# Kernel tuning notes

Measured on AMD Instinct MI355X. Metric: run time of the kernel, lower is better.

The kernel has to match this reference:

```python
import jax, jax.numpy as jnp
import numpy as np

N_NODES = 100000
IN_CH = 64
HID = 128
N_EDGES = 1600000


def sage_conv(x, src, dst, Wl, bl, Wr, num_nodes):
    # PyG SAGEConv (mean aggr): out = lin_l(mean_{j->i} x_j) + lin_r(x_i)
    msg = x[src]                                           # [E, F] gather
    agg = jax.ops.segment_sum(msg, dst, num_segments=num_nodes)   # [N, F]
    cnt = jax.ops.segment_sum(jnp.ones((src.shape[0],), x.dtype), dst,
                              num_segments=num_nodes)      # [N]
    mean = agg / jnp.maximum(cnt, 1.0)[:, None]
    return mean @ Wl.T + bl + x @ Wr.T


def setup_inputs() -> dict:
    key = jax.random.key(0)
    k1, k2, k3, k4, k5, k6, k7, k8 = jax.random.split(key, 8)
    x = jax.random.normal(k1, (N_NODES, IN_CH), dtype=jnp.float32)
    edge_index = jax.random.randint(k2, (2, N_EDGES), 0, N_NODES, dtype=jnp.int64)
    s1 = 1.0 / np.sqrt(IN_CH)
    s2 = 1.0 / np.sqrt(HID)
    Wl1 = jax.random.uniform(k3, (HID, IN_CH), jnp.float32, -s1, s1)
    bl1 = jax.random.uniform(k4, (HID,), jnp.float32, -s1, s1)
    Wr1 = jax.random.uniform(k5, (HID, IN_CH), jnp.float32, -s1, s1)
    Wl2 = jax.random.uniform(k6, (HID, HID), jnp.float32, -s2, s2)
    bl2 = jax.random.uniform(k7, (HID,), jnp.float32, -s2, s2)
    Wr2 = jax.random.uniform(k8, (HID, HID), jnp.float32, -s2, s2)
    return {"x": x, "edge_index": edge_index,
            "Wl1": Wl1, "bl1": bl1, "Wr1": Wr1,
            "Wl2": Wl2, "bl2": bl2, "Wr2": Wr2}


def reference(x, edge_index, Wl1, bl1, Wr1, Wl2, bl2, Wr2):
    src, dst = edge_index[0], edge_index[1]
    n = x.shape[0]
    h = sage_conv(x, src, dst, Wl1, bl1, Wr1, n)
    h = jax.nn.relu(h)
    # dropout p=0.2 is identity in eval/reference mode
    out = sage_conv(h, src, dst, Wl2, bl2, Wr2, n)
    return out
```

## Files before the change

### kernel.cpp

```cpp
#include <hip/hip_runtime.h>
#include <hip/hip_bf16.h>
#include <stdint.h>

#define NN 100000
#define EE 1600000
#define NBUCK 196
#define CSB 512

typedef __attribute__((ext_vector_type(4))) float f32x4;
typedef __attribute__((ext_vector_type(8))) short bf16x8;

__device__ inline ushort f2bf(float f) {
    union { float f; uint32_t u; } v; v.f = f;
    uint32_t u = v.u;
    uint32_t r = (u + 0x7fffu + ((u >> 16) & 1u)) >> 16;
    return (ushort)r;
}
__device__ inline float bflo(uint32_t u) {
    union { uint32_t u; float f; } v; v.u = u << 16; return v.f;
}
__device__ inline float bfhi(uint32_t u) {
    union { uint32_t u; float f; } v; v.u = u & 0xffff0000u; return v.f;
}

__global__ __launch_bounds__(256) void prep_kernel(
    const float* __restrict__ x, const unsigned int* __restrict__ raw,
    const float* __restrict__ Wl1, const float* __restrict__ Wr1,
    const float* __restrict__ Wl2, const float* __restrict__ Wr2,
    ushort* __restrict__ xb, ushort* __restrict__ wc1, ushort* __restrict__ wc2,
    int* __restrict__ flag, int* __restrict__ ccnt, int* __restrict__ cfill)
{
    const int gid = blockIdx.x * 256 + threadIdx.x;
    const int stride = gridDim.x * 256;

    if (gid < 4096) {
        if (raw[2 * gid + 1] != 0u) atomicOr(flag, 1);
    }
    if (gid >= 4096 && gid < 4096 + NBUCK) ccnt[gid - 4096] = 0;
    if (gid >= 4096 + NBUCK && gid < 4096 + 2 * NBUCK) cfill[gid - 4096 - NBUCK] = 0;

    const int n4 = NN * 64 / 4;
    for (int i = gid; i < n4; i += stride) {
        float4 v = *(const float4*)&x[i * 4];
        ushort o[4] = { f2bf(v.x), f2bf(v.y), f2bf(v.z), f2bf(v.w) };
        *(uint64_t*)&xb[i * 4] = *(const uint64_t*)o;
    }
    for (int i = gid; i < 128 * 128; i += stride) {
        int o = i >> 7, k = i & 127;
        float v = (k < 64) ? Wl1[o * 64 + k] : Wr1[o * 64 + (k - 64)];
        wc1[o * 128 + k] = f2bf(v);
    }
    for (int i = gid; i < 128 * 256; i += stride) {
        int o = i >> 8, k = i & 255;
        float v = (k < 128) ? Wl2[o * 128 + k] : Wr2[o * 128 + (k - 128)];
        wc2[o * 256 + k] = f2bf(v);
    }
}

__global__ __launch_bounds__(256) void coarse_hist(const void* raw, const int* flag,
                                                   int* ccnt, int E) {
    __shared__ int lh[NBUCK];
    for (int i = threadIdx.x; i < NBUCK; i += 256) lh[i] = 0;
    __syncthreads();
    int stride = gridDim.x * 256;
    if (*flag) {
        const int* p = (const int*)raw;
        for (int e = blockIdx.x * 256 + threadIdx.x; e < E; e += stride)
            atomicAdd(&lh[p[E + e] >> 9], 1);
    } else {
        const long long* p = (const long long*)raw;
        for (int e = blockIdx.x * 256 + threadIdx.x; e < E; e += stride)
            atomicAdd(&lh[((int)p[E + e]) >> 9], 1);
    }
    __syncthreads();
    for (int i = threadIdx.x; i < NBUCK; i += 256)
        if (lh[i]) atomicAdd(&ccnt[i], lh[i]);
}

__global__ void coarse_scan(const int* ccnt, int* coff, int* offsets, int E) {
    __shared__ int part[256];
    int t = threadIdx.x;
    int v[4]; int s = 0;
    #pragma unroll
    for (int j = 0; j < 4; j++) {
        int i = t * 4 + j;
        v[j] = (i < NBUCK) ? ccnt[i] : 0;
        s += v[j];
    }
    part[t] = s; __syncthreads();
    for (int off = 1; off < 256; off <<= 1) {
        int add = (t >= off) ? part[t - off] : 0;
        __syncthreads();
        part[t] += add;
        __syncthreads();
    }
    int run = part[t] - s;
    #pragma unroll
    for (int j = 0; j < 4; j++) {
        int i = t * 4 + j;
        if (i <= NBUCK) coff[i] = run;
        run += v[j];
    }
    if (t == 0) offsets[NN] = E;
}

__global__ __launch_bounds__(256) void coarse_scatter2(const void* raw, const int* flag,
                                                       const int* coff, int* cfill,
                                                       uint32_t* pbuf, int E) {
    __shared__ int lh[NBUCK];
    __shared__ int gbase[NBUCK];
    __shared__ int lfill[NBUCK];
    const int t = threadIdx.x;
    for (int i = t; i < NBUCK; i += 256) { lh[i] = 0; lfill[i] = 0; }
    __syncthreads();
    const int chunk = (E + (int)gridDim.x - 1) / (int)gridDim.x;
    const int s0 = blockIdx.x * chunk;
    const int s1 = min(E, s0 + chunk);
    const bool is32 = (*flag != 0);
    if (is32) {
        const int* p = (const int*)raw;
        for (int e = s0 + t; e < s1; e += 256) atomicAdd(&lh[p[E + e] >> 9], 1);
    } else {
        const long long* p = (const long long*)raw;
        for (int e = s0 + t; e < s1; e += 256) atomicAdd(&lh[((int)p[E + e]) >> 9], 1);
    }
    __syncthreads();
    for (int i = t; i < NBUCK; i += 256)
        gbase[i] = coff[i] + (lh[i] ? atomicAdd(&cfill[i], lh[i]) : 0);
    __syncthreads();
    if (is32) {
        const int* p = (const int*)raw;
        for (int e = s0 + t; e < s1; e += 256) {
            int sr = p[e], d = p[E + e];
            int b = d >> 9;
            int r = atomicAdd(&lfill[b], 1);
            pbuf[gbase[b] + r] = ((uint32_t)(d & 511) << 17) | (uint32_t)sr;
        }
    } else {
        const long long* p = (const long long*)raw;
        for (int e = s0 + t; e < s1; e += 256) {
            int sr = (int)p[e], d = (int)p[E + e];
            int b = d >> 9;
            int r = atomicAdd(&lfill[b], 1);
            pbuf[gbase[b] + r] = ((uint32_t)(d & 511) << 17) | (uint32_t)sr;
        }
    }
}

__global__ __launch_bounds__(512) void fine_bucket(const uint32_t* __restrict__ pbuf,
                                                   const int* __restrict__ coff,
                                                   int* __restrict__ offsets,
                                                   int* __restrict__ srcs_sort, int N) {
    __shared__ int cnt[512], sc[512], fil[512];
    const int b = blockIdx.x, t = threadIdx.x;
    const int s = coff[b], e = coff[b + 1];
    cnt[t] = 0; fil[t] = 0;
    __syncthreads();
    for (int i = s + t; i < e; i += 512) atomicAdd(&cnt[pbuf[i] >> 17], 1);
    __syncthreads();
    sc[t] = cnt[t];
    __syncthreads();
    for (int off = 1; off < 512; off <<= 1) {
        int add = (t >= off) ? sc[t - off] : 0;
        __syncthreads();
        sc[t] += add;
        __syncthreads();
    }
    const int nb0 = b * 512;
    if (nb0 + t < N) offsets[nb0 + t] = s + sc[t] - cnt[t];
    for (int i = s + t; i < e; i += 512) {
        uint32_t p = pbuf[i];
        int dl = (int)(p >> 17);
        int sr = (int)(p & 0x1FFFFu);
        int pos = s + (sc[dl] - cnt[dl]) + atomicAdd(&fil[dl], 1);
        srcs_sort[pos] = sr;
    }
}

template<int K, bool RELU, bool OUT_BF16>
__global__ __launch_bounds__(256, 8) void sage_fused(
    const int* __restrict__ offsets, const int* __restrict__ srcs,
    const ushort* __restrict__ xin, const ushort* __restrict__ Wcat,
    const float* __restrict__ bl, void* __restrict__ outv, int N)
{
    constexpr int KT = 2 * K;
    constexpr int RP = K + 8;
    __shared__ ushort mlds[32][RP];
    const int t = threadIdx.x;
    const int w = t >> 6;
    const int lane = t & 63;
    const int nb = blockIdx.x * 32;

    const int q     = lane >> 4;
    const int ql    = lane & 15;
    const int qbase = lane & 48;

    int offv = 0;
    if (lane < 9) offv = offsets[nb + w * 8 + lane];

    for (int pi = 0; pi < 2; pi++) {
        const int ln = w * 8 + pi * 4 + q;
        const int s0 = __shfl(offv, pi * 4 + q);
        const int s1 = __shfl(offv, pi * 4 + q + 1);
        const float inv = 1.0f / fmaxf((float)(s1 - s0), 1.0f);

        if (K == 64) {
            float f0=0.f, f1=0.f, f2=0.f, f3=0.f;
            for (int base = s0; base < s1; base += 16) {
                int cnt = min(16, s1 - base);
                int myidx = (base + ql < s1) ? srcs[base + ql] : 0;
                int j = 0;
                for (; j + 4 <= cnt; j += 4) {
                    int sA = __shfl(myidx, qbase + j);
                    int sB = __shfl(myidx, qbase + j + 1);
                    int sC = __shfl(myidx, qbase + j + 2);
                    int sD = __shfl(myidx, qbase + j + 3);
                    uint2 uA = *(const uint2*)&xin[(size_t)sA * 64 + ql * 4];
                    uint2 uB = *(const uint2*)&xin[(size_t)sB * 64 + ql * 4];
                    uint2 uC = *(const uint2*)&xin[(size_t)sC * 64 + ql * 4];
                    uint2 uD = *(const uint2*)&xin[(size_t)sD * 64 + ql * 4];
                    f0 += bflo(uA.x); f1 += bfhi(uA.x); f2 += bflo(uA.y); f3 += bfhi(uA.y);
                    f0 += bflo(uB.x); f1 += bfhi(uB.x); f2 += bflo(uB.y); f3 += bfhi(uB.y);
                    f0 += bflo(uC.x); f1 += bfhi(uC.x); f2 += bflo(uC.y); f3 += bfhi(uC.y);
                    f0 += bflo(uD.x); f1 += bfhi(uD.x); f2 += bflo(uD.y); f3 += bfhi(uD.y);
                }
                for (; j < cnt; j++) {
                    int s = __shfl(myidx, qbase + j);
                    uint2 u = *(const uint2*)&xin[(size_t)s * 64 + ql * 4];
                    f0 += bflo(u.x); f1 += bfhi(u.x); f2 += bflo(u.y); f3 += bfhi(u.y);
                }
            }
            ushort o[4] = { f2bf(f0 * inv), f2bf(f1 * inv), f2bf(f2 * inv), f2bf(f3 * inv) };
            *(uint64_t*)&mlds[ln][ql * 4] = *(const uint64_t*)o;
        } else {
            float f0=0.f, f1=0.f, f2=0.f, f3=0.f, f4=0.f, f5=0.f, f6=0.f, f7=0.f;
            for (int base = s0; base < s1; base += 16) {
                int cnt = min(16, s1 - base);
                int myidx = (base + ql < s1) ? srcs[base + ql] : 0;
                int j = 0;
                for (; j + 4 <= cnt; j += 4) {
                    int sA = __shfl(myidx, qbase + j);
                    int sB = __shfl(myidx, qbase + j + 1);
                    int sC = __shfl(myidx, qbase + j + 2);
                    int sD = __shfl(myidx, qbase + j + 3);
                    uint4 uA = *(const uint4*)&xin[(size_t)sA * 128 + ql * 8];
                    uint4 uB = *(const uint4*)&xin[(size_t)sB * 128 + ql * 8];
                    uint4 uC = *(const uint4*)&xin[(size_t)sC * 128 + ql * 8];
                    uint4 uD = *(const uint4*)&xin[(size_t)sD * 128 + ql * 8];
                    f0 += bflo(uA.x); f1 += bfhi(uA.x); f2 += bflo(uA.y); f3 += bfhi(uA.y);
                    f4 += bflo(uA.z); f5 += bfhi(uA.z); f6 += bflo(uA.w); f7 += bfhi(uA.w);
                    f0 += bflo(uB.x); f1 += bfhi(uB.x); f2 += bflo(uB.y); f3 += bfhi(uB.y);
                    f4 += bflo(uB.z); f5 += bfhi(uB.z); f6 += bflo(uB.w); f7 += bfhi(uB.w);
                    f0 += bflo(uC.x); f1 += bfhi(uC.x); f2 += bflo(uC.y); f3 += bfhi(uC.y);
                    f4 += bflo(uC.z); f5 += bfhi(uC.z); f6 += bflo(uC.w); f7 += bfhi(uC.w);
                    f0 += bflo(uD.x); f1 += bfhi(uD.x); f2 += bflo(uD.y); f3 += bfhi(uD.y);
                    f4 += bflo(uD.z); f5 += bfhi(uD.z); f6 += bflo(uD.w); f7 += bfhi(uD.w);
                }
                for (; j < cnt; j++) {
                    int s = __shfl(myidx, qbase + j);
                    uint4 u = *(const uint4*)&xin[(size_t)s * 128 + ql * 8];
                    f0 += bflo(u.x); f1 += bfhi(u.x); f2 += bflo(u.y); f3 += bfhi(u.y);
                    f4 += bflo(u.z); f5 += bfhi(u.z); f6 += bflo(u.w); f7 += bfhi(u.w);
                }
            }
            ushort o[8] = { f2bf(f0 * inv), f2bf(f1 * inv), f2bf(f2 * inv), f2bf(f3 * inv),
                            f2bf(f4 * inv), f2bf(f5 * inv), f2bf(f6 * inv), f2bf(f7 * inv) };
            *(uint4*)&mlds[ln][ql * 8] = *(const uint4*)o;
        }
    }
    __syncthreads();

    const int lrow = lane & 15;
    const int lgrp = lane >> 4;
    f32x4 acc[2][2];
    #pragma unroll
    for (int nt = 0; nt < 2; nt++)
        #pragma unroll
        for (int ct = 0; ct < 2; ct++)
            acc[nt][ct] = (f32x4){0.f, 0.f, 0.f, 0.f};

    #pragma unroll
    for (int ks = 0; ks < KT; ks += 32) {
        bf16x8 x0, x1;
        if (ks < K) {
            x0 = *(const bf16x8*)&mlds[lrow][ks + lgrp * 8];
            x1 = *(const bf16x8*)&mlds[16 + lrow][ks + lgrp * 8];
        } else {
            const int ac = ks - K;
            x0 = *(const bf16x8*)&xin[(size_t)(nb + lrow) * K + ac + lgrp * 8];
            x1 = *(const bf16x8*)&xin[(size_t)(nb + 16 + lrow) * K + ac + lgrp * 8];
        }
        bf16x8 wA = *(const bf16x8*)&Wcat[(size_t)(w * 32 + lrow) * KT + ks + lgrp * 8];
        bf16x8 wB = *(const bf16x8*)&Wcat[(size_t)(w * 32 + 16 + lrow) * KT + ks + lgrp * 8];
        acc[0][0] = __builtin_amdgcn_mfma_f32_16x16x32_bf16(wA, x0, acc[0][0], 0, 0, 0);
        acc[0][1] = __builtin_amdgcn_mfma_f32_16x16x32_bf16(wB, x0, acc[0][1], 0, 0, 0);
        acc[1][0] = __builtin_amdgcn_mfma_f32_16x16x32_bf16(wA, x1, acc[1][0], 0, 0, 0);
        acc[1][1] = __builtin_amdgcn_mfma_f32_16x16x32_bf16(wB, x1, acc[1][1], 0, 0, 0);
    }

    #pragma unroll
    for (int ct = 0; ct < 2; ct++) {
        const int ch0 = w * 32 + ct * 16 + lgrp * 4;
        float4 b4 = *(const float4*)&bl[ch0];
        #pragma unroll
        for (int nt = 0; nt < 2; nt++) {
            int n = nb + nt * 16 + lrow;
            float v0 = acc[nt][ct][0] + b4.x;
            float v1 = acc[nt][ct][1] + b4.y;
            float v2 = acc[nt][ct][2] + b4.z;
            float v3 = acc[nt][ct][3] + b4.w;
            if (RELU) {
                v0 = fmaxf(v0, 0.f); v1 = fmaxf(v1, 0.f);
                v2 = fmaxf(v2, 0.f); v3 = fmaxf(v3, 0.f);
            }
            if (OUT_BF16) {
                ushort o[4] = { f2bf(v0), f2bf(v1), f2bf(v2), f2bf(v3) };
                *(uint64_t*)&((ushort*)outv)[(size_t)n * 128 + ch0] = *(const uint64_t*)o;
            } else {
                float4 o = make_float4(v0, v1, v2, v3);
                *(float4*)&((float*)outv)[(size_t)n * 128 + ch0] = o;
            }
        }
    }
}

extern "C" void kernel_launch(void* const* d_in, const int* in_sizes, int n_in,
                              void* d_out, int out_size, void* d_ws, size_t ws_size,
                              hipStream_t stream) {
    const float* x   = (const float*)d_in[0];
    const void*  er  = d_in[1];
    const float* Wl1 = (const float*)d_in[2];
    const float* bl1 = (const float*)d_in[3];
    const float* Wr1 = (const float*)d_in[4];
    const float* Wl2 = (const float*)d_in[5];
    const float* bl2 = (const float*)d_in[6];
    const float* Wr2 = (const float*)d_in[7];
    float* out = (float*)d_out;

    const int N = NN, E = EE;

    char* ws = (char*)d_ws;
    size_t off = 0;
    auto carve = [&](size_t bytes) { char* p = ws + off; off += (bytes + 511) & ~(size_t)511; return p; };
    int*      flag      = (int*)     carve(4);
    int*      ccnt      = (int*)     carve((size_t)NBUCK * 4);
    int*      cfill     = (int*)     carve((size_t)NBUCK * 4);
    int*      coff      = (int*)     carve((size_t)(NBUCK + 1) * 4);
    uint32_t* pbuf      = (uint32_t*)carve((size_t)E * 4);
    int*      offsets   = (int*)     carve((size_t)(N + 1) * 4);
    int*      srcs_sort = (int*)     carve((size_t)E * 4);
    ushort*   xb        = (ushort*)  carve((size_t)N * 64 * 2);
    ushort*   hb        = (ushort*)  carve((size_t)N * 128 * 2);
    ushort*   wc1       = (ushort*)  carve((size_t)128 * 128 * 2);
    ushort*   wc2       = (ushort*)  carve((size_t)128 * 256 * 2);
    (void)ws_size;

    hipMemsetAsync(flag, 0, 4, stream);

    prep_kernel<<<2048, 256, 0, stream>>>(x, (const unsigned int*)er,
                                          Wl1, Wr1, Wl2, Wr2,
                                          xb, wc1, wc2, flag, ccnt, cfill);

    coarse_hist<<<512, 256, 0, stream>>>(er, flag, ccnt, E);
    coarse_scan<<<1, 256, 0, stream>>>(ccnt, coff, offsets, E);
    coarse_scatter2<<<CSB, 256, 0, stream>>>(er, flag, coff, cfill, pbuf, E);
    fine_bucket<<<NBUCK, 512, 0, stream>>>(pbuf, coff, offsets, srcs_sort, N);

    const int fb = N / 32;

    sage_fused<64, true, true><<<fb, 256, 0, stream>>>(offsets, srcs_sort, xb, wc1, bl1, hb, N);
    sage_fused<128, false, false><<<fb, 256, 0, stream>>>(offsets, srcs_sort, hb, wc2, bl2, out, N);
}
```

Before: 205.7 us.

## Scatter edges into fixed-capacity buckets and drop the coarse histogram pass

```diff
diff --git a/kernel.cpp b/kernel.cpp
--- a/kernel.cpp
+++ b/kernel.cpp
@@ -6,6 +6,7 @@
 #define EE 1600000
 #define NBUCK 196
 #define CSB 512
+#define CAP 12288
 
 typedef __attribute__((ext_vector_type(4))) float f32x4;
 typedef __attribute__((ext_vector_type(8))) short bf16x8;
@@ -24,20 +25,16 @@
 }
 
 __global__ __launch_bounds__(256) void prep_kernel(
-    const float* __restrict__ x, const unsigned int* __restrict__ raw,
+    const float* __restrict__ x,
     const float* __restrict__ Wl1, const float* __restrict__ Wr1,
     const float* __restrict__ Wl2, const float* __restrict__ Wr2,
     ushort* __restrict__ xb, ushort* __restrict__ wc1, ushort* __restrict__ wc2,
-    int* __restrict__ flag, int* __restrict__ ccnt, int* __restrict__ cfill)
+    int* __restrict__ cfill)
 {
     const int gid = blockIdx.x * 256 + threadIdx.x;
     const int stride = gridDim.x * 256;
 
-    if (gid < 4096) {
-        if (raw[2 * gid + 1] != 0u) atomicOr(flag, 1);
-    }
-    if (gid >= 4096 && gid < 4096 + NBUCK) ccnt[gid - 4096] = 0;
-    if (gid >= 4096 + NBUCK && gid < 4096 + 2 * NBUCK) cfill[gid - 4096 - NBUCK] = 0;
+    if (gid < NBUCK) cfill[gid] = 0;
 
     const int n4 = NN * 64 / 4;
     for (int i = gid; i < n4; i += stride) {
@@ -57,78 +54,44 @@
     }
 }
 
-__global__ __launch_bounds__(256) void coarse_hist(const void* raw, const int* flag,
-                                                   int* ccnt, int E) {
-    __shared__ int lh[NBUCK];
-    for (int i = threadIdx.x; i < NBUCK; i += 256) lh[i] = 0;
-    __syncthreads();
-    int stride = gridDim.x * 256;
-    if (*flag) {
-        const int* p = (const int*)raw;
-        for (int e = blockIdx.x * 256 + threadIdx.x; e < E; e += stride)
-            atomicAdd(&lh[p[E + e] >> 9], 1);
-    } else {
-        const long long* p = (const long long*)raw;
-        for (int e = blockIdx.x * 256 + threadIdx.x; e < E; e += stride)
-            atomicAdd(&lh[((int)p[E + e]) >> 9], 1);
-    }
-    __syncthreads();
-    for (int i = threadIdx.x; i < NBUCK; i += 256)
-        if (lh[i]) atomicAdd(&ccnt[i], lh[i]);
-}
-
-__global__ void coarse_scan(const int* ccnt, int* coff, int* offsets, int E) {
-    __shared__ int part[256];
-    int t = threadIdx.x;
-    int v[4]; int s = 0;
-    #pragma unroll
-    for (int j = 0; j < 4; j++) {
-        int i = t * 4 + j;
-        v[j] = (i < NBUCK) ? ccnt[i] : 0;
-        s += v[j];
-    }
-    part[t] = s; __syncthreads();
-    for (int off = 1; off < 256; off <<= 1) {
-        int add = (t >= off) ? part[t - off] : 0;
-        __syncthreads();
-        part[t] += add;
-        __syncthreads();
-    }
-    int run = part[t] - s;
-    #pragma unroll
-    for (int j = 0; j < 4; j++) {
-        int i = t * 4 + j;
-        if (i <= NBUCK) coff[i] = run;
-        run += v[j];
-    }
-    if (t == 0) offsets[NN] = E;
-}
-
-__global__ __launch_bounds__(256) void coarse_scatter2(const void* raw, const int* flag,
-                                                       const int* coff, int* cfill,
-                                                       uint32_t* pbuf, int E) {
+__global__ __launch_bounds__(256) void scatter_fixed(const void* raw, int* cfill,
+                                                     uint32_t* pbuf, int E) {
     __shared__ int lh[NBUCK];
     __shared__ int gbase[NBUCK];
     __shared__ int lfill[NBUCK];
+    __shared__ int is64;
     const int t = threadIdx.x;
     for (int i = t; i < NBUCK; i += 256) { lh[i] = 0; lfill[i] = 0; }
+    if (t == 0) is64 = 1;
     __syncthreads();
     const int chunk = (E + (int)gridDim.x - 1) / (int)gridDim.x;
     const int s0 = blockIdx.x * chunk;
     const int s1 = min(E, s0 + chunk);
-    const bool is32 = (*flag != 0);
-    if (is32) {
+    if (t < 64 && s0 + t < E) {
+        if (((const unsigned int*)raw)[2 * (s0 + t) + 1] != 0u) atomicAnd(&is64, 0);
+    }
+    __syncthreads();
+    const bool i64 = (is64 != 0);
+    if (i64) {
+        const long long* p = (const long long*)raw;
+        for (int e = s0 + t; e < s1; e += 256) atomicAdd(&lh[((int)p[E + e]) >> 9], 1);
+    } else {
         const int* p = (const int*)raw;
         for (int e = s0 + t; e < s1; e += 256) atomicAdd(&lh[p[E + e] >> 9], 1);
+    }
+    __syncthreads();
+    for (int i = t; i < NBUCK; i += 256)
+        gbase[i] = i * CAP + (lh[i] ? atomicAdd(&cfill[i], lh[i]) : 0);
+    __syncthreads();
+    if (i64) {
+        const long long* p = (const long long*)raw;
+        for (int e = s0 + t; e < s1; e += 256) {
+            int sr = (int)p[e], d = (int)p[E + e];
+            int b = d >> 9;
+            int r = atomicAdd(&lfill[b], 1);
+            pbuf[gbase[b] + r] = ((uint32_t)(d & 511) << 17) | (uint32_t)sr;
+        }
     } else {
-        const long long* p = (const long long*)raw;
-        for (int e = s0 + t; e < s1; e += 256) atomicAdd(&lh[((int)p[E + e]) >> 9], 1);
-    }
-    __syncthreads();
-    for (int i = t; i < NBUCK; i += 256)
-        gbase[i] = coff[i] + (lh[i] ? atomicAdd(&cfill[i], lh[i]) : 0);
-    __syncthreads();
-    if (is32) {
         const int* p = (const int*)raw;
         for (int e = s0 + t; e < s1; e += 256) {
             int sr = p[e], d = p[E + e];
@@ -136,27 +99,38 @@
             int r = atomicAdd(&lfill[b], 1);
             pbuf[gbase[b] + r] = ((uint32_t)(d & 511) << 17) | (uint32_t)sr;
         }
-    } else {
-        const long long* p = (const long long*)raw;
-        for (int e = s0 + t; e < s1; e += 256) {
-            int sr = (int)p[e], d = (int)p[E + e];
-            int b = d >> 9;
-            int r = atomicAdd(&lfill[b], 1);
-            pbuf[gbase[b] + r] = ((uint32_t)(d & 511) << 17) | (uint32_t)sr;
-        }
-    }
+    }
+}
+
+__global__ void bucket_scan(const int* __restrict__ cfill, int* __restrict__ coff,
+                            int* __restrict__ offsets, int E) {
+    __shared__ int part[256];
+    int t = threadIdx.x;
+    int v = (t < NBUCK) ? cfill[t] : 0;
+    part[t] = v; __syncthreads();
+    for (int off = 1; off < 256; off <<= 1) {
+        int add = (t >= off) ? part[t - off] : 0;
+        __syncthreads();
+        part[t] += add;
+        __syncthreads();
+    }
+    if (t < NBUCK) coff[t] = part[t] - v;
+    if (t == 0) { coff[NBUCK] = E; offsets[NN] = E; }
 }
 
 __global__ __launch_bounds__(512) void fine_bucket(const uint32_t* __restrict__ pbuf,
+                                                   const int* __restrict__ cfill,
                                                    const int* __restrict__ coff,
                                                    int* __restrict__ offsets,
                                                    int* __restrict__ srcs_sort, int N) {
     __shared__ int cnt[512], sc[512], fil[512];
     const int b = blockIdx.x, t = threadIdx.x;
-    const int s = coff[b], e = coff[b + 1];
+    const int base = b * CAP;
+    const int m = cfill[b];
+    const int s = coff[b];
     cnt[t] = 0; fil[t] = 0;
     __syncthreads();
-    for (int i = s + t; i < e; i += 512) atomicAdd(&cnt[pbuf[i] >> 17], 1);
+    for (int i = t; i < m; i += 512) atomicAdd(&cnt[pbuf[base + i] >> 17], 1);
     __syncthreads();
     sc[t] = cnt[t];
     __syncthreads();
@@ -168,12 +142,11 @@
     }
     const int nb0 = b * 512;
     if (nb0 + t < N) offsets[nb0 + t] = s + sc[t] - cnt[t];
-    for (int i = s + t; i < e; i += 512) {
-        uint32_t p = pbuf[i];
+    for (int i = t; i < m; i += 512) {
+        uint32_t p = pbuf[base + i];
         int dl = (int)(p >> 17);
-        int sr = (int)(p & 0x1FFFFu);
         int pos = s + (sc[dl] - cnt[dl]) + atomicAdd(&fil[dl], 1);
-        srcs_sort[pos] = sr;
+        srcs_sort[pos] = (int)(p & 0x1FFFFu);
     }
 }
 
@@ -342,11 +315,9 @@
     char* ws = (char*)d_ws;
     size_t off = 0;
     auto carve = [&](size_t bytes) { char* p = ws + off; off += (bytes + 511) & ~(size_t)511; return p; };
-    int*      flag      = (int*)     carve(4);
-    int*      ccnt      = (int*)     carve((size_t)NBUCK * 4);
     int*      cfill     = (int*)     carve((size_t)NBUCK * 4);
     int*      coff      = (int*)     carve((size_t)(NBUCK + 1) * 4);
-    uint32_t* pbuf      = (uint32_t*)carve((size_t)E * 4);
+    uint32_t* pbuf      = (uint32_t*)carve((size_t)NBUCK * CAP * 4);
     int*      offsets   = (int*)     carve((size_t)(N + 1) * 4);
     int*      srcs_sort = (int*)     carve((size_t)E * 4);
     ushort*   xb        = (ushort*)  carve((size_t)N * 64 * 2);
@@ -355,16 +326,11 @@
     ushort*   wc2       = (ushort*)  carve((size_t)128 * 256 * 2);
     (void)ws_size;
 
-    hipMemsetAsync(flag, 0, 4, stream);
-
-    prep_kernel<<<2048, 256, 0, stream>>>(x, (const unsigned int*)er,
-                                          Wl1, Wr1, Wl2, Wr2,
-                                          xb, wc1, wc2, flag, ccnt, cfill);
-
-    coarse_hist<<<512, 256, 0, stream>>>(er, flag, ccnt, E);
-    coarse_scan<<<1, 256, 0, stream>>>(ccnt, coff, offsets, E);
-    coarse_scatter2<<<CSB, 256, 0, stream>>>(er, flag, coff, cfill, pbuf, E);
-    fine_bucket<<<NBUCK, 512, 0, stream>>>(pbuf, coff, offsets, srcs_sort, N);
+    prep_kernel<<<2048, 256, 0, stream>>>(x, Wl1, Wr1, Wl2, Wr2, xb, wc1, wc2, cfill);
+
+    scatter_fixed<<<CSB, 256, 0, stream>>>(er, cfill, pbuf, E);
+    bucket_scan<<<1, 256, 0, stream>>>(cfill, coff, offsets, E);
+    fine_bucket<<<NBUCK, 512, 0, stream>>>(pbuf, cfill, coff, offsets, srcs_sort, N);
 
     const int fb = N / 32;
 
```

Result: faster. 186.6 us (-9.3%).
